# Performance work log

Measured on AMD Instinct MI355X. Metric: run time of the kernel, lower is better.

Reference implementation:

```python
import jax, jax.numpy as jnp
import numpy as np

N = 10000        # nodes
E = 160000       # edges
IN = 1024        # in_channels
OUT = 512        # out_channels
H = 2 * OUT      # hidden width of conv1
EPS = 1e-5
NEG_SLOPE = 0.1


def setup_inputs() -> dict:
    key = jax.random.key(0)
    ks = jax.random.split(key, 8)
    s_in = 1.0 / np.sqrt(IN)
    s_h = 1.0 / np.sqrt(H)
    return {
        "x": jax.random.normal(ks[0], (N, IN), jnp.float32),
        "edge_index": jax.random.randint(ks[1], (2, E), 0, N, dtype=jnp.int64),
        "W1": jax.random.normal(ks[2], (IN, H), jnp.float32) * s_in,
        "b1": jnp.zeros((H,), jnp.float32),
        "Wm": jax.random.normal(ks[3], (H, OUT), jnp.float32) * s_h,
        "bm": jnp.zeros((OUT,), jnp.float32),
        "Ws": jax.random.normal(ks[4], (H, OUT), jnp.float32) * s_h,
        "bs": jnp.zeros((OUT,), jnp.float32),
        "gn_weight": jnp.ones((IN,), jnp.float32),
        "gn_bias": jnp.zeros((IN,), jnp.float32),
        "gn_mean_scale": jnp.ones((IN,), jnp.float32),
    }


def reference(x, edge_index, W1, b1, Wm, bm, Ws, bs, gn_weight, gn_bias, gn_mean_scale):
    # --- GraphNorm (eval, single graph: stats over all nodes) ---
    mean = jnp.mean(x, axis=0)                       # [IN]
    xc = x - gn_mean_scale * mean                    # [N, IN]
    var = jnp.mean(xc * xc, axis=0)                  # [IN]
    x = xc * jax.lax.rsqrt(var + EPS) * gn_weight + gn_bias

    # --- GCN normalization: add self loops, symmetric degree norm ---
    loop = jnp.arange(N, dtype=edge_index.dtype)
    src = jnp.concatenate([edge_index[0], loop])     # [E+N]
    dst = jnp.concatenate([edge_index[1], loop])     # [E+N]
    deg = jax.ops.segment_sum(jnp.ones_like(dst, dtype=x.dtype), dst, num_segments=N)
    deg_inv_sqrt = jax.lax.rsqrt(deg)                # deg >= 1 due to self loops
    enorm = deg_inv_sqrt[src] * deg_inv_sqrt[dst]    # [E+N]

    def gcn_conv(h, W, b):
        h = h @ W                                                        # dense GEMM
        agg = jax.ops.segment_sum(h[src] * enorm[:, None], dst, num_segments=N)
        return agg + b

    h = jax.nn.leaky_relu(gcn_conv(x, W1, b1), NEG_SLOPE)                # [N, H]
    mu = gcn_conv(h, Wm, bm)                                             # [N, OUT]
    logstd = gcn_conv(h, Ws, bs)                                         # [N, OUT]
    z = mu  # eval-mode reparametrize returns mu
    return (z, mu, logstd)
```

## Files before the change

kernel.cpp:

```cpp
#include <hip/hip_runtime.h>
#include <hip/hip_bf16.h>
#include <stdint.h>

#define NNODES 10000
#define NEDGES 160000
#define INCH 1024
#define HCH 1024
#define OUTCH 512
#define MPAD 10112
#define EPSV 1e-5f
#define NEG 0.1f

typedef unsigned short u16;
typedef __bf16 bf16x8 __attribute__((ext_vector_type(8)));
typedef float f32x4 __attribute__((ext_vector_type(4)));
typedef __attribute__((address_space(1))) unsigned int gu32;
typedef __attribute__((address_space(3))) unsigned int lu32;

#define GL16(g, l) __builtin_amdgcn_global_load_lds((const gu32*)(g), (lu32*)(l), 16, 0, 0)

__device__ __forceinline__ float bf2f(u16 u) {
    union { unsigned int i; float f; } v; v.i = ((unsigned int)u) << 16; return v.f;
}
__device__ __forceinline__ u16 f2bf(float f) {
    union { float f; unsigned int i; } v; v.f = f;
    unsigned int r = v.i + 0x7fffu + ((v.i >> 16) & 1u);
    return (u16)(r >> 16);
}

__global__ void colsum_k(const float* __restrict__ x, float* __restrict__ colsum) {
    int c = blockIdx.x * 256 + threadIdx.x;
    int r0 = blockIdx.y * 157;
    int r1 = min(r0 + 157, NNODES);
    float s = 0.f;
    for (int r = r0; r < r1; ++r) s += x[(size_t)r * INCH + c];
    atomicAdd(&colsum[c], s);
}

__global__ void colvar_k(const float* __restrict__ x, const float* __restrict__ colsum,
                         const float* __restrict__ gms, float* __restrict__ varsum) {
    int c = blockIdx.x * 256 + threadIdx.x;
    float mean = colsum[c] * (1.0f / NNODES);
    float sub = gms[c] * mean;
    int r0 = blockIdx.y * 157;
    int r1 = min(r0 + 157, NNODES);
    float s = 0.f;
    for (int r = r0; r < r1; ++r) { float d = x[(size_t)r * INCH + c] - sub; s += d * d; }
    atomicAdd(&varsum[c], s);
}

__global__ void norm_k(const float* __restrict__ x, const float* __restrict__ colsum,
                       const float* __restrict__ varsum, const float* __restrict__ gms,
                       const float* __restrict__ gw, const float* __restrict__ gb,
                       u16* __restrict__ xn) {
    int gid = blockIdx.x * 256 + threadIdx.x;
    int e = gid * 4;
    int c = e & (INCH - 1);
    float4 xv = *(const float4*)(x + e);
    float4 cs = *(const float4*)(colsum + c);
    float4 vs = *(const float4*)(varsum + c);
    float4 g4 = *(const float4*)(gms + c);
    float4 w4 = *(const float4*)(gw + c);
    float4 b4 = *(const float4*)(gb + c);
    const float invn = 1.0f / NNODES;
    ushort4 o;
    float m, sc, val;
    m = cs.x * invn; sc = rsqrtf(vs.x * invn + EPSV) * w4.x; val = (xv.x - g4.x * m) * sc + b4.x; o.x = f2bf(val);
    m = cs.y * invn; sc = rsqrtf(vs.y * invn + EPSV) * w4.y; val = (xv.y - g4.y * m) * sc + b4.y; o.y = f2bf(val);
    m = cs.z * invn; sc = rsqrtf(vs.z * invn + EPSV) * w4.z; val = (xv.z - g4.z * m) * sc + b4.z; o.z = f2bf(val);
    m = cs.w * invn; sc = rsqrtf(vs.w * invn + EPSV) * w4.w; val = (xv.w - g4.w * m) * sc + b4.w; o.w = f2bf(val);
    *(ushort4*)(xn + e) = o;
}

__global__ void wt1_k(const float* __restrict__ W, u16* __restrict__ Bt) {
    int gid = blockIdx.x * 256 + threadIdx.x;
    int ccol = gid >> 10;
    int k = gid & 1023;
    Bt[gid] = f2bf(W[(size_t)k * HCH + ccol]);
}
__global__ void wt2_k(const float* __restrict__ Wm, const float* __restrict__ Ws,
                      u16* __restrict__ Bt) {
    int gid = blockIdx.x * 256 + threadIdx.x;
    int ccol = gid >> 10;
    int k = gid & 1023;
    float v = (ccol < OUTCH) ? Wm[(size_t)k * OUTCH + ccol]
                             : Ws[(size_t)k * OUTCH + (ccol - OUTCH)];
    Bt[gid] = f2bf(v);
}

__global__ void deg_k(const int* __restrict__ dst, int* __restrict__ cnt) {
    int e = blockIdx.x * 256 + threadIdx.x;
    if (e < NEDGES) atomicAdd(&cnt[dst[e]], 1);
}
__global__ void dis_k(const int* __restrict__ cnt, float* __restrict__ dis) {
    int i = blockIdx.x * 256 + threadIdx.x;
    if (i < NNODES) dis[i] = rsqrtf((float)(cnt[i] + 1));
}
__global__ void scan_k(const int* __restrict__ cnt, int* __restrict__ row_ptr,
                       int* __restrict__ cursor) {
    __shared__ int sm[256];
    int tid = threadIdx.x;
    const int per = 40;
    int base = tid * per;
    int s = 0;
    for (int i = 0; i < per; ++i) { int idx = base + i; if (idx < NNODES) s += cnt[idx]; }
    sm[tid] = s; __syncthreads();
    for (int off = 1; off < 256; off <<= 1) {
        int v = (tid >= off) ? sm[tid - off] : 0;
        __syncthreads();
        sm[tid] += v;
        __syncthreads();
    }
    int run = (tid == 0) ? 0 : sm[tid - 1];
    for (int i = 0; i < per; ++i) {
        int idx = base + i;
        if (idx < NNODES) { row_ptr[idx] = run; cursor[idx] = run; run += cnt[idx]; }
    }
    if (tid == 255) row_ptr[NNODES] = sm[255];
}
__global__ void fill_k(const int* __restrict__ src, const int* __restrict__ dst,
                       const float* __restrict__ dis, int* __restrict__ cursor,
                       int* __restrict__ csr_src, float* __restrict__ csr_w) {
    int e = blockIdx.x * 256 + threadIdx.x;
    if (e >= NEDGES) return;
    int s = src[e], d = dst[e];
    int pos = atomicAdd(&cursor[d], 1);
    csr_src[pos] = s;
    csr_w[pos] = dis[s] * dis[d];
}

template<int MODE>
__global__ void agg_k(const u16* __restrict__ in, u16* __restrict__ out,
                      const int* __restrict__ row_ptr, const int* __restrict__ csr_src,
                      const float* __restrict__ csr_w, const float* __restrict__ dis,
                      const float* __restrict__ bias) {
    int node = blockIdx.x;
    int c = threadIdx.x * 4;
    float dv = dis[node];
    float selfw = dv * dv;
    ushort4 sv = *(const ushort4*)(in + (size_t)node * HCH + c);
    float a0 = bf2f(sv.x) * selfw, a1 = bf2f(sv.y) * selfw;
    float a2 = bf2f(sv.z) * selfw, a3 = bf2f(sv.w) * selfw;
    int e0 = row_ptr[node], e1 = row_ptr[node + 1];
    for (int e = e0; e < e1; ++e) {
        int s = csr_src[e];
        float w = csr_w[e];
        ushort4 v = *(const ushort4*)(in + (size_t)s * HCH + c);
        a0 += bf2f(v.x) * w; a1 += bf2f(v.y) * w;
        a2 += bf2f(v.z) * w; a3 += bf2f(v.w) * w;
    }
    if (MODE == 1) {
        float4 b = *(const float4*)(bias + c);
        a0 += b.x; a1 += b.y; a2 += b.z; a3 += b.w;
        a0 = a0 > 0.f ? a0 : NEG * a0;
        a1 = a1 > 0.f ? a1 : NEG * a1;
        a2 = a2 > 0.f ? a2 : NEG * a2;
        a3 = a3 > 0.f ? a3 : NEG * a3;
    }
    ushort4 o; o.x = f2bf(a0); o.y = f2bf(a1); o.z = f2bf(a2); o.w = f2bf(a3);
    *(ushort4*)(out + (size_t)node * HCH + c) = o;
}

template<int EPI>
__global__ __launch_bounds__(256) void gemm_k(
    const u16* __restrict__ A, const u16* __restrict__ Bt,
    u16* __restrict__ Cbf, float* __restrict__ out,
    const float* __restrict__ bm, const float* __restrict__ bs) {
    __shared__ u16 As[128 * 32];
    __shared__ u16 Bs[128 * 32];
    const int tid = threadIdx.x;
    const int wave = tid >> 6;
    const int lane = tid & 63;
    const int row0 = blockIdx.y * 128;
    const int col0 = blockIdx.x * 128;
    const int wr = wave >> 1, wc = wave & 1;
    const int sr = lane >> 2;
    const int sc = (lane & 3) * 8;
    u16* AsW0 = &As[(wave * 16) * 32];
    u16* AsW1 = &As[(64 + wave * 16) * 32];
    u16* BsW0 = &Bs[(wave * 16) * 32];
    u16* BsW1 = &Bs[(64 + wave * 16) * 32];
    const u16* Ag0 = A + (size_t)(row0 + wave * 16 + sr) * 1024 + sc;
    const u16* Ag1 = A + (size_t)(row0 + 64 + wave * 16 + sr) * 1024 + sc;
    const u16* Bg0 = Bt + (size_t)(col0 + wave * 16 + sr) * 1024 + sc;
    const u16* Bg1 = Bt + (size_t)(col0 + 64 + wave * 16 + sr) * 1024 + sc;

    f32x4 acc[4][4] = {};
    const int arow = lane & 15;
    const int ak = (lane >> 4) * 8;
    for (int kk = 0; kk < 1024; kk += 32) {
        GL16(Ag0 + kk, AsW0);
        GL16(Ag1 + kk, AsW1);
        GL16(Bg0 + kk, BsW0);
        GL16(Bg1 + kk, BsW1);
        __syncthreads();
        bf16x8 af[4], bf[4];
#pragma unroll
        for (int m = 0; m < 4; ++m)
            af[m] = *reinterpret_cast<const bf16x8*>(&As[(wr * 64 + m * 16 + arow) * 32 + ak]);
#pragma unroll
        for (int n = 0; n < 4; ++n)
            bf[n] = *reinterpret_cast<const bf16x8*>(&Bs[(wc * 64 + n * 16 + arow) * 32 + ak]);
#pragma unroll
        for (int m = 0; m < 4; ++m)
#pragma unroll
            for (int n = 0; n < 4; ++n)
                acc[m][n] = __builtin_amdgcn_mfma_f32_16x16x32_bf16(af[m], bf[n], acc[m][n], 0, 0, 0);
        __syncthreads();
    }
    const int crow = (lane >> 4) * 4;
    const int ccol = lane & 15;
    if (EPI == 0) {
#pragma unroll
        for (int m = 0; m < 4; ++m) {
            int rbase = row0 + wr * 64 + m * 16 + crow;
#pragma unroll
            for (int n = 0; n < 4; ++n) {
                int col = col0 + wc * 64 + n * 16 + ccol;
                f32x4 v = acc[m][n];
#pragma unroll
                for (int r = 0; r < 4; ++r)
                    Cbf[(size_t)(rbase + r) * 1024 + col] = f2bf(v[r]);
            }
        }
    } else {
        const size_t NOUT = (size_t)NNODES * OUTCH;
#pragma unroll
        for (int n = 0; n < 4; ++n) {
            int col = col0 + wc * 64 + n * 16 + ccol;
            bool lo = col < OUTCH;
            int colo = lo ? col : col - OUTCH;
            float bias = lo ? bm[colo] : bs[colo];
#pragma unroll
            for (int m = 0; m < 4; ++m) {
                int rbase = row0 + wr * 64 + m * 16 + crow;
                f32x4 v = acc[m][n];
#pragma unroll
                for (int r = 0; r < 4; ++r) {
                    int rr = rbase + r;
                    if (rr < NNODES) {
                        float val = v[r] + bias;
                        if (lo) {
                            out[(size_t)rr * OUTCH + colo] = val;
                            out[NOUT + (size_t)rr * OUTCH + colo] = val;
                        } else {
                            out[2 * NOUT + (size_t)rr * OUTCH + colo] = val;
                        }
                    }
                }
            }
        }
    }
}

extern "C" void kernel_launch(void* const* d_in, const int* in_sizes, int n_in,
                              void* d_out, int out_size, void* d_ws, size_t ws_size,
                              hipStream_t stream) {
    const float* x   = (const float*)d_in[0];
    const int*   ei  = (const int*)d_in[1];
    const float* W1  = (const float*)d_in[2];
    const float* b1  = (const float*)d_in[3];
    const float* Wm  = (const float*)d_in[4];
    const float* bm  = (const float*)d_in[5];
    const float* Ws  = (const float*)d_in[6];
    const float* bs  = (const float*)d_in[7];
    const float* gw  = (const float*)d_in[8];
    const float* gb  = (const float*)d_in[9];
    const float* gms = (const float*)d_in[10];
    const int* srcI = ei;
    const int* dstI = ei + NEDGES;

    char* ws = (char*)d_ws;
    const size_t SBIG = (size_t)MPAD * 1024 * 2;
    u16* xn   = (u16*)(ws);
    u16* h1g  = (u16*)(ws + SBIG);
    u16* h    = (u16*)(ws + 2 * SBIG);
    u16* aggh = xn;
    u16* Bt1  = (u16*)(ws + 3 * SBIG);
    u16* Bt2  = (u16*)(ws + 3 * SBIG + (size_t)2 * 1024 * 1024);
    char* small   = ws + 3 * SBIG + (size_t)4 * 1024 * 1024;
    float* colsum = (float*)(small);
    float* varsum = (float*)(small + 4096);
    int*   cnt    = (int*)(small + 8192);
    int*   row_ptr= (int*)(small + 49152);
    int*   cursor = (int*)(small + 49152 + 40960);
    float* dis    = (float*)(small + 49152 + 81920);
    int*   csr_src= (int*)(small + 49152 + 122880);
    float* csr_w  = (float*)(small + 49152 + 122880 + 640000);

    hipMemsetAsync(small, 0, 48192, stream);

    colsum_k<<<dim3(4, 64), 256, 0, stream>>>(x, colsum);
    colvar_k<<<dim3(4, 64), 256, 0, stream>>>(x, colsum, gms, varsum);
    norm_k<<<10000, 256, 0, stream>>>(x, colsum, varsum, gms, gw, gb, xn);
    wt1_k<<<4096, 256, 0, stream>>>(W1, Bt1);
    wt2_k<<<4096, 256, 0, stream>>>(Wm, Ws, Bt2);
    deg_k<<<625, 256, 0, stream>>>(dstI, cnt);
    dis_k<<<40, 256, 0, stream>>>(cnt, dis);
    scan_k<<<1, 256, 0, stream>>>(cnt, row_ptr, cursor);
    fill_k<<<625, 256, 0, stream>>>(srcI, dstI, dis, cursor, csr_src, csr_w);

    gemm_k<0><<<dim3(8, 79), 256, 0, stream>>>(xn, Bt1, h1g, nullptr, nullptr, nullptr);
    agg_k<1><<<NNODES, 256, 0, stream>>>(h1g, h, row_ptr, csr_src, csr_w, dis, b1);
    agg_k<0><<<NNODES, 256, 0, stream>>>(h, aggh, row_ptr, csr_src, csr_w, dis, nullptr);
    gemm_k<1><<<dim3(8, 79), 256, 0, stream>>>(aggh, Bt2, nullptr, (float*)d_out, bm, bs);
}
```

Measured before the change: 453.3 us.

## Fuse GraphNorm stats into one pass and tile weight transposes through LDS

Replaces the separate column-sum and centered-variance passes over x with a single pass that accumulates sum and sum of squares, then computes the variance algebraically in a small scale kernel that precomputes per-column scale and shift. The norm kernel then applies a single fused multiply-add per element. The weight transpose kernels are rewritten to use 64x64 LDS tiles with coalesced float4 reads and ushort4 writes instead of strided scalar gathers. The one-pass variance formula can lose precision when the mean is large relative to the spread.

```diff
diff --git a/kernel.cpp b/kernel.cpp
--- a/kernel.cpp
+++ b/kernel.cpp
@@ -28,64 +28,110 @@
     return (u16)(r >> 16);
 }
 
-__global__ void colsum_k(const float* __restrict__ x, float* __restrict__ colsum) {
+__global__ __launch_bounds__(256) void sumsq_k(const float* __restrict__ x,
+                                               float* __restrict__ colsum,
+                                               float* __restrict__ colsq) {
+    int c = threadIdx.x * 4;
+    int r0 = blockIdx.x * 16;
+    float s0 = 0.f, s1 = 0.f, s2 = 0.f, s3 = 0.f;
+    float q0 = 0.f, q1 = 0.f, q2 = 0.f, q3 = 0.f;
+#pragma unroll 4
+    for (int r = 0; r < 16; ++r) {
+        float4 v = *(const float4*)(x + (size_t)(r0 + r) * INCH + c);
+        s0 += v.x; s1 += v.y; s2 += v.z; s3 += v.w;
+        q0 += v.x * v.x; q1 += v.y * v.y; q2 += v.z * v.z; q3 += v.w * v.w;
+    }
+    atomicAdd(&colsum[c + 0], s0); atomicAdd(&colsum[c + 1], s1);
+    atomicAdd(&colsum[c + 2], s2); atomicAdd(&colsum[c + 3], s3);
+    atomicAdd(&colsq[c + 0], q0); atomicAdd(&colsq[c + 1], q1);
+    atomicAdd(&colsq[c + 2], q2); atomicAdd(&colsq[c + 3], q3);
+}
+
+__global__ void scale_k(const float* __restrict__ colsum, const float* __restrict__ colsq,
+                        const float* __restrict__ gms, const float* __restrict__ gw,
+                        const float* __restrict__ gb,
+                        float* __restrict__ sc, float* __restrict__ sh) {
     int c = blockIdx.x * 256 + threadIdx.x;
-    int r0 = blockIdx.y * 157;
-    int r1 = min(r0 + 157, NNODES);
-    float s = 0.f;
-    for (int r = r0; r < r1; ++r) s += x[(size_t)r * INCH + c];
-    atomicAdd(&colsum[c], s);
-}
-
-__global__ void colvar_k(const float* __restrict__ x, const float* __restrict__ colsum,
-                         const float* __restrict__ gms, float* __restrict__ varsum) {
-    int c = blockIdx.x * 256 + threadIdx.x;
-    float mean = colsum[c] * (1.0f / NNODES);
-    float sub = gms[c] * mean;
-    int r0 = blockIdx.y * 157;
-    int r1 = min(r0 + 157, NNODES);
-    float s = 0.f;
-    for (int r = r0; r < r1; ++r) { float d = x[(size_t)r * INCH + c] - sub; s += d * d; }
-    atomicAdd(&varsum[c], s);
-}
-
-__global__ void norm_k(const float* __restrict__ x, const float* __restrict__ colsum,
-                       const float* __restrict__ varsum, const float* __restrict__ gms,
-                       const float* __restrict__ gw, const float* __restrict__ gb,
-                       u16* __restrict__ xn) {
+    const float invn = 1.0f / NNODES;
+    float m = colsum[c] * invn;
+    float msq = colsq[c] * invn;
+    float g = gms[c];
+    float var = msq - g * (2.0f - g) * m * m;
+    float s = rsqrtf(var + EPSV) * gw[c];
+    sc[c] = s;
+    sh[c] = gb[c] - g * m * s;
+}
+
+__global__ __launch_bounds__(256) void norm_k(const float* __restrict__ x,
+                                              const float* __restrict__ sc,
+                                              const float* __restrict__ sh,
+                                              u16* __restrict__ xn) {
     int gid = blockIdx.x * 256 + threadIdx.x;
     int e = gid * 4;
     int c = e & (INCH - 1);
     float4 xv = *(const float4*)(x + e);
-    float4 cs = *(const float4*)(colsum + c);
-    float4 vs = *(const float4*)(varsum + c);
-    float4 g4 = *(const float4*)(gms + c);
-    float4 w4 = *(const float4*)(gw + c);
-    float4 b4 = *(const float4*)(gb + c);
-    const float invn = 1.0f / NNODES;
+    float4 s4 = *(const float4*)(sc + c);
+    float4 h4 = *(const float4*)(sh + c);
     ushort4 o;
-    float m, sc, val;
-    m = cs.x * invn; sc = rsqrtf(vs.x * invn + EPSV) * w4.x; val = (xv.x - g4.x * m) * sc + b4.x; o.x = f2bf(val);
-    m = cs.y * invn; sc = rsqrtf(vs.y * invn + EPSV) * w4.y; val = (xv.y - g4.y * m) * sc + b4.y; o.y = f2bf(val);
-    m = cs.z * invn; sc = rsqrtf(vs.z * invn + EPSV) * w4.z; val = (xv.z - g4.z * m) * sc + b4.z; o.z = f2bf(val);
-    m = cs.w * invn; sc = rsqrtf(vs.w * invn + EPSV) * w4.w; val = (xv.w - g4.w * m) * sc + b4.w; o.w = f2bf(val);
+    o.x = f2bf(xv.x * s4.x + h4.x);
+    o.y = f2bf(xv.y * s4.y + h4.y);
+    o.z = f2bf(xv.z * s4.z + h4.z);
+    o.w = f2bf(xv.w * s4.w + h4.w);
     *(ushort4*)(xn + e) = o;
 }
 
-__global__ void wt1_k(const float* __restrict__ W, u16* __restrict__ Bt) {
-    int gid = blockIdx.x * 256 + threadIdx.x;
-    int ccol = gid >> 10;
-    int k = gid & 1023;
-    Bt[gid] = f2bf(W[(size_t)k * HCH + ccol]);
-}
-__global__ void wt2_k(const float* __restrict__ Wm, const float* __restrict__ Ws,
-                      u16* __restrict__ Bt) {
-    int gid = blockIdx.x * 256 + threadIdx.x;
-    int ccol = gid >> 10;
-    int k = gid & 1023;
-    float v = (ccol < OUTCH) ? Wm[(size_t)k * OUTCH + ccol]
-                             : Ws[(size_t)k * OUTCH + (ccol - OUTCH)];
-    Bt[gid] = f2bf(v);
+__global__ __launch_bounds__(256) void wt1_k(const float* __restrict__ W, u16* __restrict__ Bt) {
+    __shared__ u16 t[64][68];
+    int k0 = blockIdx.y * 64, c0 = blockIdx.x * 64;
+    int tc = (threadIdx.x & 15) * 4;
+    int tk = threadIdx.x >> 4;
+#pragma unroll
+    for (int i = 0; i < 64; i += 16) {
+        float4 v = *(const float4*)(W + (size_t)(k0 + tk + i) * HCH + c0 + tc);
+        t[tc + 0][tk + i] = f2bf(v.x);
+        t[tc + 1][tk + i] = f2bf(v.y);
+        t[tc + 2][tk + i] = f2bf(v.z);
+        t[tc + 3][tk + i] = f2bf(v.w);
+    }
+    __syncthreads();
+    int wk = (threadIdx.x & 15) * 4;
+    int wc = threadIdx.x >> 4;
+#pragma unroll
+    for (int i = 0; i < 64; i += 16) {
+        ushort4 o;
+        o.x = t[wc + i][wk + 0]; o.y = t[wc + i][wk + 1];
+        o.z = t[wc + i][wk + 2]; o.w = t[wc + i][wk + 3];
+        *(ushort4*)(Bt + (size_t)(c0 + wc + i) * 1024 + k0 + wk) = o;
+    }
+}
+
+__global__ __launch_bounds__(256) void wt2_k(const float* __restrict__ Wm,
+                                             const float* __restrict__ Ws,
+                                             u16* __restrict__ Bt) {
+    __shared__ u16 t[64][68];
+    int k0 = blockIdx.y * 64, c0 = blockIdx.x * 64;
+    const float* W = (c0 < OUTCH) ? Wm : Ws;
+    int cb = (c0 < OUTCH) ? c0 : c0 - OUTCH;
+    int tc = (threadIdx.x & 15) * 4;
+    int tk = threadIdx.x >> 4;
+#pragma unroll
+    for (int i = 0; i < 64; i += 16) {
+        float4 v = *(const float4*)(W + (size_t)(k0 + tk + i) * OUTCH + cb + tc);
+        t[tc + 0][tk + i] = f2bf(v.x);
+        t[tc + 1][tk + i] = f2bf(v.y);
+        t[tc + 2][tk + i] = f2bf(v.z);
+        t[tc + 3][tk + i] = f2bf(v.w);
+    }
+    __syncthreads();
+    int wk = (threadIdx.x & 15) * 4;
+    int wc = threadIdx.x >> 4;
+#pragma unroll
+    for (int i = 0; i < 64; i += 16) {
+        ushort4 o;
+        o.x = t[wc + i][wk + 0]; o.y = t[wc + i][wk + 1];
+        o.z = t[wc + i][wk + 2]; o.w = t[wc + i][wk + 3];
+        *(ushort4*)(Bt + (size_t)(c0 + wc + i) * 1024 + k0 + wk) = o;
+    }
 }
 
 __global__ void deg_k(const int* __restrict__ dst, int* __restrict__ cnt) {
@@ -280,21 +326,23 @@
     u16* Bt2  = (u16*)(ws + 3 * SBIG + (size_t)2 * 1024 * 1024);
     char* small   = ws + 3 * SBIG + (size_t)4 * 1024 * 1024;
     float* colsum = (float*)(small);
-    float* varsum = (float*)(small + 4096);
+    float* colsq  = (float*)(small + 4096);
     int*   cnt    = (int*)(small + 8192);
     int*   row_ptr= (int*)(small + 49152);
     int*   cursor = (int*)(small + 49152 + 40960);
     float* dis    = (float*)(small + 49152 + 81920);
     int*   csr_src= (int*)(small + 49152 + 122880);
     float* csr_w  = (float*)(small + 49152 + 122880 + 640000);
+    float* sc     = (float*)(small + 49152 + 122880 + 1280000);
+    float* sh     = (float*)(small + 49152 + 122880 + 1280000 + 4096);
 
     hipMemsetAsync(small, 0, 48192, stream);
 
-    colsum_k<<<dim3(4, 64), 256, 0, stream>>>(x, colsum);
-    colvar_k<<<dim3(4, 64), 256, 0, stream>>>(x, colsum, gms, varsum);
-    norm_k<<<10000, 256, 0, stream>>>(x, colsum, varsum, gms, gw, gb, xn);
-    wt1_k<<<4096, 256, 0, stream>>>(W1, Bt1);
-    wt2_k<<<4096, 256, 0, stream>>>(Wm, Ws, Bt2);
+    sumsq_k<<<625, 256, 0, stream>>>(x, colsum, colsq);
+    scale_k<<<4, 256, 0, stream>>>(colsum, colsq, gms, gw, gb, sc, sh);
+    norm_k<<<10000, 256, 0, stream>>>(x, sc, sh, xn);
+    wt1_k<<<dim3(16, 16), 256, 0, stream>>>(W1, Bt1);
+    wt2_k<<<dim3(16, 16), 256, 0, stream>>>(Wm, Ws, Bt2);
     deg_k<<<625, 256, 0, stream>>>(dstI, cnt);
     dis_k<<<40, 256, 0, stream>>>(cnt, dis);
     scan_k<<<1, 256, 0, stream>>>(cnt, row_ptr, cursor);
```

Measured after the change: 415.1 us. 1.09x faster.
